# Performance work log

Measured on AMD Instinct MI355X. Metric: run time of the kernel, lower is better.

Reference implementation:

```python
import jax, jax.numpy as jnp
import numpy as np

TEMP = 0.07
NUM_CLASSES = 4

def setup_inputs() -> dict:
    key = jax.random.key(0)
    k1, k2 = jax.random.split(key)
    features_in = jax.random.normal(k1, (4, 64, 2048), dtype=jnp.float32)
    labels_in = jax.random.randint(k2, (4, 2048), 0, NUM_CLASSES, dtype=jnp.int64)
    return {"features_in": features_in, "labels_in": labels_in}

def reference(features_in, labels_in):
    B, C, N = features_in.shape
    M = B * N
    # torch .view(C, B*N): row-major reinterpret of contiguous [B,C,N]
    feats = features_in.reshape(C, M).T            # [M, C]
    labels = labels_in.reshape(-1)                 # [M]

    # per-class keep probability: min(750/(count+1), 1), gathered by label
    counts = jnp.bincount(labels, length=NUM_CLASSES)
    keep_p = jnp.minimum(750.0 / (counts.astype(jnp.float32) + 1.0), 1.0)
    p = keep_p[labels]                             # [M]
    sel = jax.random.bernoulli(jax.random.key(42), p)  # [M] bool, stochastic subsample

    # L2 normalize rows; original divides by norms of already-normalized rows (==1)
    nv = feats / jnp.linalg.norm(feats, axis=1, keepdims=True)
    sim = nv @ nv.T                                # [M, M] cosine similarities
    dp = jnp.exp(sim / TEMP)
    dp = dp * (1.0 - jnp.eye(M, dtype=dp.dtype))   # zero the diagonal

    same = labels[:, None] == labels[None, :]
    pair = sel[:, None] & sel[None, :]             # both points kept
    pos = jnp.sum(jnp.where(same & pair, dp, 0.0), axis=1)
    neg = jnp.sum(jnp.where((~same) & pair, dp, 0.0), axis=1)

    frac = pos / (pos + neg)
    per = -jnp.log(jnp.where(sel, frac, 1.0))      # guard unselected rows
    n_sel = jnp.maximum(jnp.sum(sel), 1)
    loss = jnp.sum(jnp.where(sel, per, 0.0)) / n_sel
    return loss
```

## Files before the change

### kernel.cpp

```cpp
#include <hip/hip_runtime.h>
#include <hip/hip_bf16.h>

#define M_TOT 8192
#define NCLS 4
#define NSEL_CAP 4096
#define NT 64

typedef __attribute__((ext_vector_type(8)))  short short8v;
typedef __attribute__((ext_vector_type(16))) float f32x16;

__device__ __forceinline__ unsigned int rotl32(unsigned int x, unsigned int r) {
    return (x << r) | (x >> (32u - r));
}

__device__ unsigned int threefry_bits_key42(unsigned int m) {
    const unsigned int ks0 = 0u;
    const unsigned int ks1 = 42u;
    const unsigned int ks2 = 0x1BD11BDAu ^ 0u ^ 42u;
    unsigned int j  = (m < 4096u) ? m : (m - 4096u);
    unsigned int x0 = j + ks0;
    unsigned int x1 = (j + 4096u) + ks1;
#define TF_RND(r) { x0 += x1; x1 = rotl32(x1, (r)); x1 ^= x0; }
    TF_RND(13u) TF_RND(15u) TF_RND(26u) TF_RND(6u)
    x0 += ks1; x1 += ks2 + 1u;
    TF_RND(17u) TF_RND(29u) TF_RND(16u) TF_RND(24u)
    x0 += ks2; x1 += ks0 + 2u;
    TF_RND(13u) TF_RND(15u) TF_RND(26u) TF_RND(6u)
    x0 += ks0; x1 += ks1 + 3u;
    TF_RND(17u) TF_RND(29u) TF_RND(16u) TF_RND(24u)
    x0 += ks1; x1 += ks2 + 4u;
    TF_RND(13u) TF_RND(15u) TF_RND(26u) TF_RND(6u)
    x0 += ks2; x1 += ks0 + 5u;
#undef TF_RND
    return (m < 4096u) ? x0 : x1;
}

__device__ __forceinline__ unsigned short f2bf(float x) {
    const unsigned int u = __float_as_uint(x);
    return (unsigned short)((u + 0x7FFFu + ((u >> 16) & 1u)) >> 16);
}
__device__ __forceinline__ float bf2f(unsigned short b) {
    return __uint_as_float(((unsigned int)b) << 16);
}

__global__ void hist_kernel(const int* __restrict__ labels,
                            int* __restrict__ hist_part,
                            float* __restrict__ pos,
                            float* __restrict__ neg) {
    __shared__ int lhist[NCLS];
    const int t = threadIdx.x;
    const int gid = blockIdx.x * 256 + t;
    for (int i = gid; i < M_TOT; i += 2048) { pos[i] = 0.0f; neg[i] = 0.0f; }
    if (t < NCLS) lhist[t] = 0;
    __syncthreads();

    const int base = blockIdx.x * 1024 + t * 4;
    int c0 = 0, c1 = 0, c2 = 0, c3 = 0;
    #pragma unroll
    for (int r = 0; r < 4; ++r) {
        const int lab = labels[base + r];
        c0 += (lab == 0); c1 += (lab == 1); c2 += (lab == 2); c3 += (lab == 3);
    }
    int cc[4] = {c0, c1, c2, c3};
    const int lane = t & 63;
    #pragma unroll
    for (int cls = 0; cls < NCLS; ++cls) {
        int v = cc[cls];
        for (int off = 32; off > 0; off >>= 1) v += __shfl_down(v, off, 64);
        if (lane == 0) atomicAdd(&lhist[cls], v);
    }
    __syncthreads();
    if (t < NCLS) hist_part[blockIdx.x * NCLS + t] = lhist[t];
}

__global__ void select_kernel(const int* __restrict__ labels,
                              const int* __restrict__ hist_part,
                              int* __restrict__ nsel_g,
                              int* __restrict__ sel_idx,
                              int* __restrict__ lab_sel) {
    __shared__ float keepp[NCLS];
    __shared__ int   wtot[4];
    const int t = threadIdx.x;
    if (t < NCLS) {
        int s = 0;
        #pragma unroll
        for (int b = 0; b < 8; ++b) s += hist_part[b * NCLS + t];
        keepp[t] = fminf(750.0f / ((float)s + 1.0f), 1.0f);
    }
    __syncthreads();

    const int m0 = t * 32;
    unsigned int flags = 0u;
    int cnt = 0;
    for (int r = 0; r < 32; ++r) {
        const int m = m0 + r;
        const unsigned int bits = threefry_bits_key42((unsigned int)m);
        const float u = __uint_as_float((bits >> 9) | 0x3F800000u) - 1.0f;
        if (u < keepp[labels[m]]) { flags |= (1u << r); ++cnt; }
    }
    const int lane = t & 63, w = t >> 6;
    int x = cnt;
    #pragma unroll
    for (int off = 1; off < 64; off <<= 1) {
        const int y = __shfl_up(x, off, 64);
        if (lane >= off) x += y;
    }
    if (lane == 63) wtot[w] = x;
    const int excl = x - cnt;
    __syncthreads();
    int base = excl;
    for (int w2 = 0; w2 < w; ++w2) base += wtot[w2];
    if (t == 0) *nsel_g = wtot[0] + wtot[1] + wtot[2] + wtot[3];
    for (int r = 0; r < 32; ++r) {
        if (flags & (1u << r)) {
            const int m = m0 + r;
            sel_idx[base] = m;
            lab_sel[base] = labels[m];
            ++base;
        }
    }
}

__global__ void norm_kernel(const float* __restrict__ features,
                            const int* __restrict__ sel_idx,
                            const int* __restrict__ nsel_g,
                            unsigned short* __restrict__ nv_hi,
                            unsigned short* __restrict__ nv_lo) {
    const int tid = blockIdx.x * 256 + threadIdx.x;
    const int p  = tid >> 3;
    const int kg = tid & 7;
    const int nsel = *nsel_g;
    const int ofs = (p << 6) + kg * 8;
    if (p >= nsel) {
        const uint4 z = {0, 0, 0, 0};
        *(uint4*)&nv_hi[ofs] = z;
        *(uint4*)&nv_lo[ofs] = z;
        return;
    }
    const int m = sel_idx[p];
    float v[8];
    float ss = 0.0f;
    #pragma unroll
    for (int q = 0; q < 8; ++q) {
        v[q] = features[(kg * 8 + q) * M_TOT + m];
        ss += v[q] * v[q];
    }
    ss += __shfl_xor(ss, 1, 8);
    ss += __shfl_xor(ss, 2, 8);
    ss += __shfl_xor(ss, 4, 8);
    const float rn = rsqrtf(ss);
    unsigned short hs[8], ls[8];
    #pragma unroll
    for (int q = 0; q < 8; ++q) {
        const float x = v[q] * rn;
        const unsigned short h = f2bf(x);
        hs[q] = h;
        ls[q] = f2bf(x - bf2f(h));
    }
    *(uint4*)&nv_hi[ofs] = *(const uint4*)hs;
    *(uint4*)&nv_lo[ofs] = *(const uint4*)ls;
}

#define EXP2_SCALE 20.609929155556605f
#define LSTR 72

__global__ __launch_bounds__(256, 4) void pair_kernel(
        const unsigned short* __restrict__ nv_hi,
        const unsigned short* __restrict__ nv_lo,
        const int* __restrict__ lab_sel,
        const int* __restrict__ nsel_g,
        float* __restrict__ pos,
        float* __restrict__ neg) {
    const int nsel = *nsel_g;
    const int it = blockIdx.y, jt = blockIdx.x;
    const int i0 = it * 64, j0 = jt * 64;
    if (i0 >= nsel || j0 >= nsel) return;

    __shared__ __align__(16) short sAhi[64][LSTR];
    __shared__ __align__(16) short sAlo[64][LSTR];
    __shared__ __align__(16) short sBhi[64][LSTR];
    __shared__ __align__(16) short sBlo[64][LSTR];
    __shared__ int La[64], Lb[64];

    const int t = threadIdx.x;
    for (int idx = t; idx < 512; idx += 256) {
        const int p  = idx >> 3;
        const int kc = (idx & 7) * 8;
        *(uint4*)&sAhi[p][kc] = *(const uint4*)&nv_hi[((i0 + p) << 6) + kc];
        *(uint4*)&sAlo[p][kc] = *(const uint4*)&nv_lo[((i0 + p) << 6) + kc];
        *(uint4*)&sBhi[p][kc] = *(const uint4*)&nv_hi[((j0 + p) << 6) + kc];
        *(uint4*)&sBlo[p][kc] = *(const uint4*)&nv_lo[((j0 + p) << 6) + kc];
    }
    if (t < 64)       La[t]      = lab_sel[i0 + t];
    else if (t < 128) Lb[t - 64] = lab_sel[j0 + t - 64];
    __syncthreads();

    const int wave = t >> 6, lane = t & 63;
    const int qi = (wave >> 1) * 32, qj = (wave & 1) * 32;
    const int half = lane >> 5, l31 = lane & 31;
    const int ra = qi + l31;
    const int rb = qj + l31;

    f32x16 acc;
    #pragma unroll
    for (int r = 0; r < 16; ++r) acc[r] = 0.0f;

    #pragma unroll
    for (int k0 = 0; k0 < 64; k0 += 16) {
        const int ka = k0 + half * 8;
        const short8v ah = *(const short8v*)&sAhi[ra][ka];
        const short8v al = *(const short8v*)&sAlo[ra][ka];
        const short8v bh = *(const short8v*)&sBhi[rb][ka];
        const short8v bl = *(const short8v*)&sBlo[rb][ka];
        acc = __builtin_amdgcn_mfma_f32_32x32x16_bf16(ah, bh, acc, 0, 0, 0);
        acc = __builtin_amdgcn_mfma_f32_32x32x16_bf16(ah, bl, acc, 0, 0, 0);
        acc = __builtin_amdgcn_mfma_f32_32x32x16_bf16(al, bh, acc, 0, 0, 0);
    }

    const int colL = qj + l31;
    const int jg = j0 + colL;
    const int Lj = Lb[colL];
    float cp = 0.0f, cn = 0.0f;
    #pragma unroll
    for (int r = 0; r < 16; ++r) {
        const int rowL = qi + (r & 3) + 8 * (r >> 2) + 4 * half;
        const int ig = i0 + rowL;
        const bool valid = (ig < nsel) && (jg < nsel) && (ig != jg);
        const float d = valid ? exp2f(acc[r] * EXP2_SCALE) : 0.0f;
        if (La[rowL] == Lj) cp += d; else cn += d;
    }
    cp += __shfl_xor(cp, 32, 64);
    cn += __shfl_xor(cn, 32, 64);
    if (half == 0 && jg < nsel) {
        atomicAdd(&pos[jg], cp);
        atomicAdd(&neg[jg], cn);
    }
}

__global__ void loss_kernel(const float* __restrict__ pos,
                            const float* __restrict__ neg,
                            const int* __restrict__ nsel_g,
                            float* __restrict__ out) {
    const int nsel = *nsel_g;
    float s = 0.0f;
    for (int i = threadIdx.x; i < nsel; i += 256) {
        const float fr = pos[i] / (pos[i] + neg[i]);
        s += -logf(fr);
    }
    __shared__ float red[256];
    red[threadIdx.x] = s;
    __syncthreads();
    for (int off = 128; off > 0; off >>= 1) {
        if (threadIdx.x < off) red[threadIdx.x] += red[threadIdx.x + off];
        __syncthreads();
    }
    if (threadIdx.x == 0) out[0] = red[0] / (float)(nsel > 0 ? nsel : 1);
}

extern "C" void kernel_launch(void* const* d_in, const int* in_sizes, int n_in,
                              void* d_out, int out_size, void* d_ws, size_t ws_size,
                              hipStream_t stream) {
    const float* features = (const float*)d_in[0];
    const int*   labels   = (const int*)d_in[1];
    float*       out      = (float*)d_out;
    char*        ws       = (char*)d_ws;

    int*   nsel_g    = (int*)(ws);
    int*   hist_part = (int*)(ws + 64);
    int*   sel_idx   = (int*)(ws + 1024);
    int*   lab_sel   = (int*)(ws + 1024 + 16384);
    float* pos       = (float*)(ws + 1024 + 32768);
    float* neg       = pos + M_TOT;
    unsigned short* nv_hi = (unsigned short*)(ws + 1024 + 32768 + 65536);
    unsigned short* nv_lo = nv_hi + NSEL_CAP * 64;

    hist_kernel<<<8, 256, 0, stream>>>(labels, hist_part, pos, neg);
    select_kernel<<<1, 256, 0, stream>>>(labels, hist_part, nsel_g, sel_idx, lab_sel);
    norm_kernel<<<128, 256, 0, stream>>>(features, sel_idx, nsel_g, nv_hi, nv_lo);
    pair_kernel<<<dim3(NT, NT), 256, 0, stream>>>(nv_hi, nv_lo, lab_sel, nsel_g, pos, neg);
    loss_kernel<<<1, 256, 0, stream>>>(pos, neg, nsel_g, out);
}
```

Measured before the change: 90.30 us.

## Fuse histogram into select, loss into pair kernel via last-block reduction

Drops the separate histogram and loss kernels. The class histogram moves into the single-block select kernel, and zeroing of pos/neg moves into the norm kernel. The final loss is computed by the last pair-kernel block to finish, detected with an atomic done counter and thread fences. It also changes the shared-memory fragment layout to a fragment-major arrangement without padding. Together these cut launch overhead and inter-kernel gaps. In exchange, every one of the 4096 pair blocks, including inactive ones, now does a fence and an atomic increment, and the tail block runs the reduction serially.

Result: slower. 335.6 us (+271.6%).

```diff
diff --git a/kernel.cpp b/kernel.cpp
--- a/kernel.cpp
+++ b/kernel.cpp
@@ -5,6 +5,7 @@
 #define NCLS 4
 #define NSEL_CAP 4096
 #define NT 64
+#define NBLOCKS (NT * NT)
 
 typedef __attribute__((ext_vector_type(8)))  short short8v;
 typedef __attribute__((ext_vector_type(16))) float f32x16;
@@ -43,53 +44,37 @@
     return __uint_as_float(((unsigned int)b) << 16);
 }
 
-__global__ void hist_kernel(const int* __restrict__ labels,
-                            int* __restrict__ hist_part,
-                            float* __restrict__ pos,
-                            float* __restrict__ neg) {
-    __shared__ int lhist[NCLS];
+__global__ void select_kernel(const int* __restrict__ labels,
+                              int* __restrict__ nsel_g,
+                              int* __restrict__ done_ctr,
+                              int* __restrict__ sel_idx,
+                              int* __restrict__ lab_sel) {
+    __shared__ int   hist[NCLS];
+    __shared__ float keepp[NCLS];
+    __shared__ int   wtot[4];
     const int t = threadIdx.x;
-    const int gid = blockIdx.x * 256 + t;
-    for (int i = gid; i < M_TOT; i += 2048) { pos[i] = 0.0f; neg[i] = 0.0f; }
-    if (t < NCLS) lhist[t] = 0;
-    __syncthreads();
-
-    const int base = blockIdx.x * 1024 + t * 4;
+    const int lane = t & 63, w = t >> 6;
+    if (t == 0) *done_ctr = 0;
+    if (t < NCLS) hist[t] = 0;
+    __syncthreads();
+
+    const int m0 = t * 32;
     int c0 = 0, c1 = 0, c2 = 0, c3 = 0;
-    #pragma unroll
-    for (int r = 0; r < 4; ++r) {
-        const int lab = labels[base + r];
+    for (int r = 0; r < 32; ++r) {
+        const int lab = labels[m0 + r];
         c0 += (lab == 0); c1 += (lab == 1); c2 += (lab == 2); c3 += (lab == 3);
     }
     int cc[4] = {c0, c1, c2, c3};
-    const int lane = t & 63;
     #pragma unroll
     for (int cls = 0; cls < NCLS; ++cls) {
         int v = cc[cls];
         for (int off = 32; off > 0; off >>= 1) v += __shfl_down(v, off, 64);
-        if (lane == 0) atomicAdd(&lhist[cls], v);
-    }
-    __syncthreads();
-    if (t < NCLS) hist_part[blockIdx.x * NCLS + t] = lhist[t];
-}
-
-__global__ void select_kernel(const int* __restrict__ labels,
-                              const int* __restrict__ hist_part,
-                              int* __restrict__ nsel_g,
-                              int* __restrict__ sel_idx,
-                              int* __restrict__ lab_sel) {
-    __shared__ float keepp[NCLS];
-    __shared__ int   wtot[4];
-    const int t = threadIdx.x;
-    if (t < NCLS) {
-        int s = 0;
-        #pragma unroll
-        for (int b = 0; b < 8; ++b) s += hist_part[b * NCLS + t];
-        keepp[t] = fminf(750.0f / ((float)s + 1.0f), 1.0f);
-    }
-    __syncthreads();
-
-    const int m0 = t * 32;
+        if (lane == 0) atomicAdd(&hist[cls], v);
+    }
+    __syncthreads();
+    if (t < NCLS) keepp[t] = fminf(750.0f / ((float)hist[t] + 1.0f), 1.0f);
+    __syncthreads();
+
     unsigned int flags = 0u;
     int cnt = 0;
     for (int r = 0; r < 32; ++r) {
@@ -98,7 +83,6 @@
         const float u = __uint_as_float((bits >> 9) | 0x3F800000u) - 1.0f;
         if (u < keepp[labels[m]]) { flags |= (1u << r); ++cnt; }
     }
-    const int lane = t & 63, w = t >> 6;
     int x = cnt;
     #pragma unroll
     for (int off = 1; off < 64; off <<= 1) {
@@ -125,8 +109,11 @@
                             const int* __restrict__ sel_idx,
                             const int* __restrict__ nsel_g,
                             unsigned short* __restrict__ nv_hi,
-                            unsigned short* __restrict__ nv_lo) {
+                            unsigned short* __restrict__ nv_lo,
+                            float* __restrict__ pos,
+                            float* __restrict__ neg) {
     const int tid = blockIdx.x * 256 + threadIdx.x;
+    if (tid < M_TOT) { pos[tid] = 0.0f; neg[tid] = 0.0f; }
     const int p  = tid >> 3;
     const int kg = tid & 7;
     const int nsel = *nsel_g;
@@ -162,7 +149,6 @@
 }
 
 #define EXP2_SCALE 20.609929155556605f
-#define LSTR 72
 
 __global__ __launch_bounds__(256, 4) void pair_kernel(
         const unsigned short* __restrict__ nv_hi,
@@ -170,91 +156,101 @@
         const int* __restrict__ lab_sel,
         const int* __restrict__ nsel_g,
         float* __restrict__ pos,
-        float* __restrict__ neg) {
+        float* __restrict__ neg,
+        int* __restrict__ done_ctr,
+        float* __restrict__ out) {
     const int nsel = *nsel_g;
     const int it = blockIdx.y, jt = blockIdx.x;
     const int i0 = it * 64, j0 = jt * 64;
-    if (i0 >= nsel || j0 >= nsel) return;
-
-    __shared__ __align__(16) short sAhi[64][LSTR];
-    __shared__ __align__(16) short sAlo[64][LSTR];
-    __shared__ __align__(16) short sBhi[64][LSTR];
-    __shared__ __align__(16) short sBlo[64][LSTR];
+    const bool active = (i0 < nsel) && (j0 < nsel);
+
+    __shared__ __align__(16) unsigned short frags[2][2][8][64][8];
     __shared__ int La[64], Lb[64];
+    __shared__ int lastflag;
 
     const int t = threadIdx.x;
-    for (int idx = t; idx < 512; idx += 256) {
-        const int p  = idx >> 3;
-        const int kc = (idx & 7) * 8;
-        *(uint4*)&sAhi[p][kc] = *(const uint4*)&nv_hi[((i0 + p) << 6) + kc];
-        *(uint4*)&sAlo[p][kc] = *(const uint4*)&nv_lo[((i0 + p) << 6) + kc];
-        *(uint4*)&sBhi[p][kc] = *(const uint4*)&nv_hi[((j0 + p) << 6) + kc];
-        *(uint4*)&sBlo[p][kc] = *(const uint4*)&nv_lo[((j0 + p) << 6) + kc];
-    }
-    if (t < 64)       La[t]      = lab_sel[i0 + t];
-    else if (t < 128) Lb[t - 64] = lab_sel[j0 + t - 64];
-    __syncthreads();
-
     const int wave = t >> 6, lane = t & 63;
-    const int qi = (wave >> 1) * 32, qj = (wave & 1) * 32;
-    const int half = lane >> 5, l31 = lane & 31;
-    const int ra = qi + l31;
-    const int rb = qj + l31;
-
-    f32x16 acc;
-    #pragma unroll
-    for (int r = 0; r < 16; ++r) acc[r] = 0.0f;
-
-    #pragma unroll
-    for (int k0 = 0; k0 < 64; k0 += 16) {
-        const int ka = k0 + half * 8;
-        const short8v ah = *(const short8v*)&sAhi[ra][ka];
-        const short8v al = *(const short8v*)&sAlo[ra][ka];
-        const short8v bh = *(const short8v*)&sBhi[rb][ka];
-        const short8v bl = *(const short8v*)&sBlo[rb][ka];
-        acc = __builtin_amdgcn_mfma_f32_32x32x16_bf16(ah, bh, acc, 0, 0, 0);
-        acc = __builtin_amdgcn_mfma_f32_32x32x16_bf16(ah, bl, acc, 0, 0, 0);
-        acc = __builtin_amdgcn_mfma_f32_32x32x16_bf16(al, bh, acc, 0, 0, 0);
-    }
-
-    const int colL = qj + l31;
-    const int jg = j0 + colL;
-    const int Lj = Lb[colL];
-    float cp = 0.0f, cn = 0.0f;
-    #pragma unroll
-    for (int r = 0; r < 16; ++r) {
-        const int rowL = qi + (r & 3) + 8 * (r >> 2) + 4 * half;
-        const int ig = i0 + rowL;
-        const bool valid = (ig < nsel) && (jg < nsel) && (ig != jg);
-        const float d = valid ? exp2f(acc[r] * EXP2_SCALE) : 0.0f;
-        if (La[rowL] == Lj) cp += d; else cn += d;
-    }
-    cp += __shfl_xor(cp, 32, 64);
-    cn += __shfl_xor(cn, 32, 64);
-    if (half == 0 && jg < nsel) {
-        atomicAdd(&pos[jg], cp);
-        atomicAdd(&neg[jg], cn);
-    }
-}
-
-__global__ void loss_kernel(const float* __restrict__ pos,
-                            const float* __restrict__ neg,
-                            const int* __restrict__ nsel_g,
-                            float* __restrict__ out) {
-    const int nsel = *nsel_g;
+
+    if (active) {
+        #pragma unroll
+        for (int it8 = 0; it8 < 8; ++it8) {
+            const int slot = it8 * 256 + t;
+            const int side  = slot >> 10;
+            const int plane = (slot >> 9) & 1;
+            const int c     = (slot >> 6) & 7;
+            const int row   = slot & 63;
+            const unsigned short* src = plane ? nv_lo : nv_hi;
+            const int basep = (side ? j0 : i0) + row;
+            const uint4 v = *(const uint4*)&src[(basep << 6) + c * 8];
+            *(uint4*)&((unsigned short*)frags)[slot * 8] = v;
+        }
+        if (t < 64)       La[t]      = lab_sel[i0 + t];
+        else if (t < 128) Lb[t - 64] = lab_sel[j0 + t - 64];
+        __syncthreads();
+
+        const int qi = (wave >> 1) * 32, qj = (wave & 1) * 32;
+        const int half = lane >> 5, l31 = lane & 31;
+        const int ra = qi + l31, rb = qj + l31;
+
+        f32x16 acc;
+        #pragma unroll
+        for (int r = 0; r < 16; ++r) acc[r] = 0.0f;
+
+        #pragma unroll
+        for (int s = 0; s < 4; ++s) {
+            const int c = 2 * s + half;
+            const short8v ah = *(const short8v*)&frags[0][0][c][ra][0];
+            const short8v al = *(const short8v*)&frags[0][1][c][ra][0];
+            const short8v bh = *(const short8v*)&frags[1][0][c][rb][0];
+            const short8v bl = *(const short8v*)&frags[1][1][c][rb][0];
+            acc = __builtin_amdgcn_mfma_f32_32x32x16_bf16(ah, bh, acc, 0, 0, 0);
+            acc = __builtin_amdgcn_mfma_f32_32x32x16_bf16(ah, bl, acc, 0, 0, 0);
+            acc = __builtin_amdgcn_mfma_f32_32x32x16_bf16(al, bh, acc, 0, 0, 0);
+        }
+
+        const int colL = qj + l31;
+        const int jg = j0 + colL;
+        const int Lj = Lb[colL];
+        float cp = 0.0f, cn = 0.0f;
+        #pragma unroll
+        for (int r = 0; r < 16; ++r) {
+            const int rowL = qi + (r & 3) + 8 * (r >> 2) + 4 * half;
+            const int ig = i0 + rowL;
+            const bool valid = (ig < nsel) && (jg < nsel) && (ig != jg);
+            const float d = valid ? exp2f(acc[r] * EXP2_SCALE) : 0.0f;
+            if (La[rowL] == Lj) cp += d; else cn += d;
+        }
+        cp += __shfl_xor(cp, 32, 64);
+        cn += __shfl_xor(cn, 32, 64);
+        if (half == 0 && jg < nsel) {
+            atomicAdd(&pos[jg], cp);
+            atomicAdd(&neg[jg], cn);
+        }
+    }
+
+    __threadfence();
+    if (t == 0) {
+        const int old = atomicAdd(done_ctr, 1);
+        lastflag = (old == NBLOCKS - 1);
+    }
+    __syncthreads();
+    if (!lastflag) return;
+
+    __threadfence();
     float s = 0.0f;
-    for (int i = threadIdx.x; i < nsel; i += 256) {
-        const float fr = pos[i] / (pos[i] + neg[i]);
-        s += -logf(fr);
-    }
-    __shared__ float red[256];
-    red[threadIdx.x] = s;
+    for (int i = t; i < nsel; i += 256) {
+        const float p = __hip_atomic_load(&pos[i], __ATOMIC_RELAXED, __HIP_MEMORY_SCOPE_AGENT);
+        const float n = __hip_atomic_load(&neg[i], __ATOMIC_RELAXED, __HIP_MEMORY_SCOPE_AGENT);
+        s += -logf(p / (p + n));
+    }
+    float* red = (float*)frags;
+    red[t] = s;
     __syncthreads();
     for (int off = 128; off > 0; off >>= 1) {
-        if (threadIdx.x < off) red[threadIdx.x] += red[threadIdx.x + off];
+        if (t < off) red[t] += red[t + off];
         __syncthreads();
     }
-    if (threadIdx.x == 0) out[0] = red[0] / (float)(nsel > 0 ? nsel : 1);
+    if (t == 0) out[0] = red[0] / (float)(nsel > 0 ? nsel : 1);
 }
 
 extern "C" void kernel_launch(void* const* d_in, const int* in_sizes, int n_in,
@@ -265,18 +261,17 @@
     float*       out      = (float*)d_out;
     char*        ws       = (char*)d_ws;
 
-    int*   nsel_g    = (int*)(ws);
-    int*   hist_part = (int*)(ws + 64);
-    int*   sel_idx   = (int*)(ws + 1024);
-    int*   lab_sel   = (int*)(ws + 1024 + 16384);
-    float* pos       = (float*)(ws + 1024 + 32768);
-    float* neg       = pos + M_TOT;
+    int*   nsel_g   = (int*)(ws);
+    int*   done_ctr = (int*)(ws + 8);
+    int*   sel_idx  = (int*)(ws + 1024);
+    int*   lab_sel  = (int*)(ws + 1024 + 16384);
+    float* pos      = (float*)(ws + 1024 + 32768);
+    float* neg      = pos + M_TOT;
     unsigned short* nv_hi = (unsigned short*)(ws + 1024 + 32768 + 65536);
     unsigned short* nv_lo = nv_hi + NSEL_CAP * 64;
 
-    hist_kernel<<<8, 256, 0, stream>>>(labels, hist_part, pos, neg);
-    select_kernel<<<1, 256, 0, stream>>>(labels, hist_part, nsel_g, sel_idx, lab_sel);
-    norm_kernel<<<128, 256, 0, stream>>>(features, sel_idx, nsel_g, nv_hi, nv_lo);
-    pair_kernel<<<dim3(NT, NT), 256, 0, stream>>>(nv_hi, nv_lo, lab_sel, nsel_g, pos, neg);
-    loss_kernel<<<1, 256, 0, stream>>>(pos, neg, nsel_g, out);
-}
+    select_kernel<<<1, 256, 0, stream>>>(labels, nsel_g, done_ctr, sel_idx, lab_sel);
+    norm_kernel<<<128, 256, 0, stream>>>(features, sel_idx, nsel_g, nv_hi, nv_lo, pos, neg);
+    pair_kernel<<<dim3(NT, NT), 256, 0, stream>>>(nv_hi, nv_lo, lab_sel, nsel_g,
+                                                  pos, neg, done_ctr, out);
+}
```
